# Kernel optimization log

Hardware: AMD Instinct MI355X
Metric: run time of the kernel (lower is better)

The kernel has to match this reference:

```python
import jax, jax.numpy as jnp
import numpy as np

DIM = 192
HEADS = 6
HEAD_DIM = DIM // HEADS
WS = 8
SHIFT = WS // 2
B, H, W = 32, 64, 64
EPS = 1e-5


def _rel_pos_index(ws):
    coords = np.stack(np.meshgrid(np.arange(ws), np.arange(ws), indexing='ij'))  # [2,ws,ws]
    cf = coords.reshape(2, -1)  # [2,N]
    rel = cf[:, :, None] - cf[:, None, :]  # [2,N,N]
    rel = rel.transpose(1, 2, 0)
    rel[:, :, 0] += ws - 1
    rel[:, :, 1] += ws - 1
    rel[:, :, 0] *= 2 * ws - 1
    return jnp.asarray(rel.sum(-1))  # [N,N] int32


def _shift_mask(Hp, Wp, ws, shift):
    img = np.zeros((Hp, Wp))
    slices = (slice(0, -ws), slice(-ws, -shift), slice(-shift, None))
    cnt = 0
    for hs in slices:
        for wsl in slices:
            img[hs, wsl] = cnt
            cnt += 1
    m = img.reshape(Hp // ws, ws, Wp // ws, ws).transpose(0, 2, 1, 3).reshape(-1, ws * ws)
    diff = m[:, None, :] - m[:, :, None]
    return jnp.asarray(np.where(diff != 0, -100.0, 0.0).astype(np.float32))  # [nW,N,N]


def _layernorm(x, g, b):
    mu = x.mean(-1, keepdims=True)
    var = ((x - mu) ** 2).mean(-1, keepdims=True)
    return (x - mu) / jnp.sqrt(var + EPS) * g + b


def _win_part(x, ws):
    b, h, w, c = x.shape
    x = x.reshape(b, h // ws, ws, w // ws, ws, c).transpose(0, 1, 3, 2, 4, 5)
    return x.reshape(-1, ws * ws, c)


def _win_rev(win, ws, h, w):
    b = win.shape[0] // (h * w // ws // ws)
    x = win.reshape(b, h // ws, w // ws, ws, ws, -1).transpose(0, 1, 3, 2, 4, 5)
    return x.reshape(b, h, w, -1)


def setup_inputs() -> dict:
    key = jax.random.key(0)
    ks = jax.random.split(key, 6)
    d = DIM
    init = lambda k, shape, scale: jax.random.normal(k, shape, jnp.float32) * scale
    return {
        'x': jax.random.normal(ks[0], (B, H, W, d), jnp.float32),
        'ln1_g': jnp.ones((d,), jnp.float32),
        'ln1_b': jnp.zeros((d,), jnp.float32),
        'qkv_w': init(ks[1], (3 * d, d), 0.02),
        'qkv_b': jnp.zeros((3 * d,), jnp.float32),
        'proj_w': init(ks[2], (d, d), 0.02),
        'proj_b': jnp.zeros((d,), jnp.float32),
        'rel_bias_table': init(ks[3], ((2 * WS - 1) ** 2, HEADS), 0.02),
        'ln2_g': jnp.ones((d,), jnp.float32),
        'ln2_b': jnp.zeros((d,), jnp.float32),
        'mlp_w1': init(ks[4], (4 * d, d), 0.02),
        'mlp_b1': jnp.zeros((4 * d,), jnp.float32),
        'mlp_w2': init(ks[5], (d, 4 * d), 0.02),
        'mlp_b2': jnp.zeros((d,), jnp.float32),
    }


def reference(x, ln1_g, ln1_b, qkv_w, qkv_b, proj_w, proj_b, rel_bias_table, ln2_g, ln2_b, mlp_w1, mlp_b1, mlp_w2, mlp_b2):
    b, h, w, c = x.shape
    N = WS * WS
    shortcut = x
    y = _layernorm(x, ln1_g, ln1_b)
    # shifted window: roll, partition
    y = jnp.roll(y, shift=(-SHIFT, -SHIFT), axis=(1, 2))
    xw = _win_part(y, WS)  # [B_, N, C]
    B_ = xw.shape[0]
    qkv = (xw @ qkv_w.T + qkv_b).reshape(B_, N, 3, HEADS, HEAD_DIM)
    q, k, v = qkv[:, :, 0], qkv[:, :, 1], qkv[:, :, 2]  # [B_, N, H, hd]
    scale = HEAD_DIM ** -0.5
    attn = jnp.einsum('bnhd,bmhd->bhnm', q * scale, k)  # [B_, H, N, N]
    rel = rel_bias_table[_rel_pos_index(WS)]  # [N, N, heads]
    attn = attn + rel.transpose(2, 0, 1)[None]
    mask = _shift_mask(h, w, WS, SHIFT)  # [nW, N, N]
    nW = mask.shape[0]
    attn = attn.reshape(B_ // nW, nW, HEADS, N, N) + mask[None, :, None]
    attn = jax.nn.softmax(attn.reshape(B_, HEADS, N, N), axis=-1)
    out = jnp.einsum('bhnm,bmhd->bnhd', attn, v).reshape(B_, N, c)
    out = out @ proj_w.T + proj_b
    y = _win_rev(out, WS, h, w)
    y = jnp.roll(y, shift=(SHIFT, SHIFT), axis=(1, 2))
    x2 = shortcut + y
    z = _layernorm(x2, ln2_g, ln2_b)
    z = jax.nn.gelu(z @ mlp_w1.T + mlp_b1, approximate=False) @ mlp_w2.T + mlp_b2
    return x2 + z
```

## Files before the change

### kernel.cpp

```cpp
#include <hip/hip_runtime.h>
#include <hip/hip_bf16.h>

typedef __bf16 bf16_t;
typedef __bf16 bf16x8 __attribute__((ext_vector_type(8)));
typedef float f32x4 __attribute__((ext_vector_type(4)));

#define MFMA16x16(a, b, c) __builtin_amdgcn_mfma_f32_16x16x32_bf16((a), (b), (c), 0, 0, 0)

constexpr int DIM = 192;
constexpr int NHEAD = 6;
constexpr int NWIN = 2048;
constexpr int WTOK = 64;

__global__ __launch_bounds__(256) void cvt_all(const float* __restrict__ qkv,
                                               const float* __restrict__ proj,
                                               const float* __restrict__ w1,
                                               const float* __restrict__ w2,
                                               bf16_t* __restrict__ qkvwf,
                                               bf16_t* __restrict__ pwf,
                                               bf16_t* __restrict__ w1f,
                                               bf16_t* __restrict__ w2f) {
    const int t = blockIdx.x * 256 + threadIdx.x;
    const int lane = t & 63;
    const int r15 = lane & 15, c8 = (lane >> 4) * 8;
    const float* sp;
    bf16_t* dp;
    if (t < 216 * 64) {
        const int f = t >> 6;
        const int nt = f & 1, kk = (f >> 1) % 6, ph = f / 12;
        sp = qkv + (ph * 32 + nt * 16 + r15) * 192 + kk * 32 + c8;
        dp = qkvwf + (size_t)t * 8;
    } else if (t < 288 * 64) {
        const int f = (t >> 6) - 216;
        const int nt = f % 3, kk = (f / 3) % 6, wv = f / 18;
        sp = proj + (wv * 48 + nt * 16 + r15) * 192 + kk * 32 + c8;
        dp = pwf + (size_t)(t - 216 * 64) * 8;
    } else if (t < 576 * 64) {
        const int f = (t >> 6) - 288;
        const int nt = f % 3, kk = (f / 3) % 6, q = f / 18;
        const int wv = q & 3, kc = q >> 2;
        sp = w1 + (kc * 192 + wv * 48 + nt * 16 + r15) * 192 + kk * 32 + c8;
        dp = w1f + (size_t)(t - 288 * 64) * 8;
    } else {
        const int f = (t >> 6) - 576;
        const int nt = f % 3, kk = (f / 3) % 6, q = f / 18;
        const int wv = q & 3, kc = q >> 2;
        sp = w2 + (size_t)(wv * 48 + nt * 16 + r15) * 768 + kc * 192 + kk * 32 + c8;
        dp = w2f + (size_t)(t - 576 * 64) * 8;
    }
#pragma unroll
    for (int e = 0; e < 8; ++e) dp[e] = (bf16_t)sp[e];
}

__global__ __launch_bounds__(256) void ln_win_kernel(const float* __restrict__ in,
                                                     const float* __restrict__ g,
                                                     const float* __restrict__ bta,
                                                     bf16_t* __restrict__ ywf) {
    __shared__ bf16_t y_s[64][200];
    const int tid = threadIdx.x, lane = tid & 63, wv = tid >> 6;
    const int win = blockIdx.x;
    const int b_ = win >> 6, hb = (win >> 3) & 7, wb = win & 7;
    const float gv0 = g[lane], gv1 = g[lane + 64], gv2 = g[lane + 128];
    const float bv0 = bta[lane], bv1 = bta[lane + 64], bv2 = bta[lane + 128];
    for (int i = 0; i < 16; ++i) {
        const int n = wv * 16 + i;
        const int th = n >> 3, tw = n & 7;
        const int hh = (hb * 8 + th + 4) & 63;
        const int ww = (wb * 8 + tw + 4) & 63;
        const size_t src = ((size_t)(b_ * 64 + hh) * 64 + ww) * DIM;
        const float v0 = in[src + lane], v1 = in[src + lane + 64], v2 = in[src + lane + 128];
        float sm = v0 + v1 + v2;
        float q = v0 * v0 + v1 * v1 + v2 * v2;
#pragma unroll
        for (int m = 1; m < 64; m <<= 1) {
            sm += __shfl_xor(sm, m);
            q += __shfl_xor(q, m);
        }
        const float mu = sm * (1.0f / DIM);
        const float inv = rsqrtf(q * (1.0f / DIM) - mu * mu + 1e-5f);
        y_s[n][lane]       = (bf16_t)((v0 - mu) * inv * gv0 + bv0);
        y_s[n][lane + 64]  = (bf16_t)((v1 - mu) * inv * gv1 + bv1);
        y_s[n][lane + 128] = (bf16_t)((v2 - mu) * inv * gv2 + bv2);
    }
    __syncthreads();
    bf16_t* dst = ywf + (size_t)win * 12288;
    for (int j = tid; j < 1536; j += 256) {
        const int f = j >> 6, ln = j & 63;
        const int mt = f & 3, kk = f >> 2;
        const int row = mt * 16 + (ln & 15), col = kk * 32 + (ln >> 4) * 8;
        *reinterpret_cast<bf16x8*>(dst + (size_t)j * 8) =
            *reinterpret_cast<const bf16x8*>(&y_s[row][col]);
    }
}

__global__ __launch_bounds__(64, 3) void attn_kernel(const bf16_t* __restrict__ ywf,
                                                     const bf16_t* __restrict__ qkvwf,
                                                     const float* __restrict__ qkvb,
                                                     const float* __restrict__ relb,
                                                     bf16_t* __restrict__ awf) {
    __shared__ bf16_t scr[6400];
    const int lane = threadIdx.x;
    const int l15 = lane & 15, l4 = lane >> 4;
    const int wh = (blockIdx.x & 7) * ((NWIN * NHEAD) >> 3) + (blockIdx.x >> 3);
    const int win = wh / 6;
    const int h = wh - win * 6;
    const bf16_t* ywin = ywf + (size_t)win * 12288;

    bf16_t* tb = scr;
    bf16_t* vtb = scr + 4096;

    f32x4 aQ[4][2] = {}, aK[4][2] = {}, aV[4][2] = {};
#pragma unroll
    for (int kk = 0; kk < 6; ++kk) {
        bf16x8 a[4];
#pragma unroll
        for (int mt = 0; mt < 4; ++mt)
            a[mt] = *reinterpret_cast<const bf16x8*>(ywin + ((kk * 4 + mt) << 9) + lane * 8);
        bf16x8 bq[2], bk2[2], bv[2];
#pragma unroll
        for (int nt = 0; nt < 2; ++nt) {
            bq[nt] = *reinterpret_cast<const bf16x8*>(
                qkvwf + (size_t)(((((h) * 6 + kk) << 1) + nt) << 9) + lane * 8);
            bk2[nt] = *reinterpret_cast<const bf16x8*>(
                qkvwf + (size_t)(((((6 + h) * 6 + kk) << 1) + nt) << 9) + lane * 8);
            bv[nt] = *reinterpret_cast<const bf16x8*>(
                qkvwf + (size_t)(((((12 + h) * 6 + kk) << 1) + nt) << 9) + lane * 8);
        }
        __builtin_amdgcn_s_setprio(1);
#pragma unroll
        for (int mt = 0; mt < 4; ++mt)
#pragma unroll
            for (int nt = 0; nt < 2; ++nt) {
                aQ[mt][nt] = MFMA16x16(a[mt], bq[nt], aQ[mt][nt]);
                aK[mt][nt] = MFMA16x16(a[mt], bk2[nt], aK[mt][nt]);
                aV[mt][nt] = MFMA16x16(a[mt], bv[nt], aV[mt][nt]);
            }
        __builtin_amdgcn_s_setprio(0);
    }

#pragma unroll
    for (int nt = 0; nt < 2; ++nt) {
        const int d = nt * 16 + l15;
        const float bias = qkvb[(12 + h) * 32 + d];
#pragma unroll
        for (int mt = 0; mt < 4; ++mt)
#pragma unroll
            for (int r = 0; r < 4; ++r)
                vtb[d * 72 + mt * 16 + l4 * 4 + r] = (bf16_t)(aV[mt][nt][r] + bias);
    }
#pragma unroll
    for (int nt = 0; nt < 2; ++nt) {
        const int d = nt * 16 + l15;
        const float bias = qkvb[h * 32 + d];
#pragma unroll
        for (int mt = 0; mt < 4; ++mt)
#pragma unroll
            for (int r = 0; r < 4; ++r)
                tb[(mt * 16 + l4 * 4 + r) * 40 + d] =
                    (bf16_t)((aQ[mt][nt][r] + bias) * 0.17677669529663689f);
    }
    bf16x8 aq[4];
#pragma unroll
    for (int mt = 0; mt < 4; ++mt)
        aq[mt] = *reinterpret_cast<const bf16x8*>(&tb[(mt * 16 + l15) * 40 + l4 * 8]);

#pragma unroll
    for (int nt = 0; nt < 2; ++nt) {
        const int d = nt * 16 + l15;
        const float bias = qkvb[(6 + h) * 32 + d];
#pragma unroll
        for (int mt = 0; mt < 4; ++mt)
#pragma unroll
            for (int r = 0; r < 4; ++r)
                tb[(mt * 16 + l4 * 4 + r) * 40 + d] = (bf16_t)(aK[mt][nt][r] + bias);
    }
    bf16x8 bk[4];
#pragma unroll
    for (int nt = 0; nt < 4; ++nt)
        bk[nt] = *reinterpret_cast<const bf16x8*>(&tb[(nt * 16 + l15) * 40 + l4 * 8]);

    f32x4 s[4][4] = {};
    __builtin_amdgcn_s_setprio(1);
#pragma unroll
    for (int mt = 0; mt < 4; ++mt)
#pragma unroll
        for (int nt = 0; nt < 4; ++nt)
            s[mt][nt] = MFMA16x16(aq[mt], bk[nt], s[mt][nt]);
    __builtin_amdgcn_s_setprio(0);

    const int hb = (win >> 3) & 7, wb = win & 7;
    int colc[4], colreg[4];
#pragma unroll
    for (int nt = 0; nt < 4; ++nt) {
        const int m = nt * 16 + l15;
        const int mh = m >> 3, mw = m & 7;
        colc[nt] = mh * 15 + mw;
        const int gh = hb * 8 + mh, gw = wb * 8 + mw;
        const int rh = (gh < 56) ? 0 : ((gh < 60) ? 1 : 2);
        const int rw = (gw < 56) ? 0 : ((gw < 60) ? 1 : 2);
        colreg[nt] = rh * 3 + rw;
    }
#pragma unroll
    for (int mt = 0; mt < 4; ++mt) {
#pragma unroll
        for (int r = 0; r < 4; ++r) {
            const int n = mt * 16 + l4 * 4 + r;
            const int nh = n >> 3, nw = n & 7;
            const int rowc = nh * 15 + nw + 112;
            const int gh = hb * 8 + nh, gw = wb * 8 + nw;
            const int rh = (gh < 56) ? 0 : ((gh < 60) ? 1 : 2);
            const int rw = (gw < 56) ? 0 : ((gw < 60) ? 1 : 2);
            const int rreg = rh * 3 + rw;
            float vals[4];
            float mx = -1e30f;
#pragma unroll
            for (int nt = 0; nt < 4; ++nt) {
                float v = s[mt][nt][r] + relb[(rowc - colc[nt]) * NHEAD + h];
                if (rreg != colreg[nt]) v -= 100.0f;
                vals[nt] = v;
                mx = fmaxf(mx, v);
            }
            mx = fmaxf(mx, __shfl_xor(mx, 1));
            mx = fmaxf(mx, __shfl_xor(mx, 2));
            mx = fmaxf(mx, __shfl_xor(mx, 4));
            mx = fmaxf(mx, __shfl_xor(mx, 8));
            float sum = 0.f;
#pragma unroll
            for (int nt = 0; nt < 4; ++nt) {
                vals[nt] = __expf(vals[nt] - mx);
                sum += vals[nt];
            }
            sum += __shfl_xor(sum, 1);
            sum += __shfl_xor(sum, 2);
            sum += __shfl_xor(sum, 4);
            sum += __shfl_xor(sum, 8);
            const float inv = 1.0f / sum;
            const int nsw = n & 7;
#pragma unroll
            for (int nt = 0; nt < 4; ++nt) {
                const int tk = nt * 16 + l15;
                tb[n * 64 + (((tk >> 3) ^ nsw) << 3) + (tk & 7)] = (bf16_t)(vals[nt] * inv);
            }
        }
    }

    f32x4 o[4][2] = {};
#pragma unroll
    for (int kk = 0; kk < 2; ++kk) {
        bf16x8 a[4], b[2];
#pragma unroll
        for (int mt = 0; mt < 4; ++mt) {
            const int tq = mt * 16 + l15;
            a[mt] = *reinterpret_cast<const bf16x8*>(&tb[tq * 64 + (((kk * 4 + l4) ^ (tq & 7)) << 3)]);
        }
#pragma unroll
        for (int nt = 0; nt < 2; ++nt)
            b[nt] = *reinterpret_cast<const bf16x8*>(&vtb[(nt * 16 + l15) * 72 + kk * 32 + l4 * 8]);
        __builtin_amdgcn_s_setprio(1);
#pragma unroll
        for (int mt = 0; mt < 4; ++mt)
#pragma unroll
            for (int nt = 0; nt < 2; ++nt)
                o[mt][nt] = MFMA16x16(a[mt], b[nt], o[mt][nt]);
        __builtin_amdgcn_s_setprio(0);
    }

#pragma unroll
    for (int mt = 0; mt < 4; ++mt)
#pragma unroll
        for (int nt = 0; nt < 2; ++nt)
#pragma unroll
            for (int r = 0; r < 4; ++r) {
                const int n = mt * 16 + l4 * 4 + r;
                tb[n * 40 + nt * 16 + l15] = (bf16_t)o[mt][nt][r];
            }
    bf16_t* op = awf + (size_t)win * 12288 + ((size_t)h << 11);
#pragma unroll
    for (int mt = 0; mt < 4; ++mt) {
        const bf16x8 v = *reinterpret_cast<const bf16x8*>(&tb[(mt * 16 + l15) * 40 + l4 * 8]);
        *reinterpret_cast<bf16x8*>(op + (mt << 9) + lane * 8) = v;
    }
}

__global__ __launch_bounds__(256) void proj_kernel(const bf16_t* __restrict__ awf,
                                                   const bf16_t* __restrict__ pwf,
                                                   const float* __restrict__ pbias,
                                                   const float* __restrict__ x,
                                                   float* __restrict__ x2) {
    const int tid = threadIdx.x;
    const int lane = tid & 63;
    const int wv = tid >> 6;
    const int win = blockIdx.x;
    const int l15 = lane & 15, l4 = lane >> 4;
    const bf16_t* awin = awf + (size_t)win * 12288;

    const int n0 = wv * 48;
    f32x4 acc[4][3] = {};
    for (int kk = 0; kk < 6; ++kk) {
        bf16x8 a[4], b[3];
#pragma unroll
        for (int mt = 0; mt < 4; ++mt)
            a[mt] = *reinterpret_cast<const bf16x8*>(awin + ((kk * 4 + mt) << 9) + lane * 8);
#pragma unroll
        for (int nt = 0; nt < 3; ++nt)
            b[nt] = *reinterpret_cast<const bf16x8*>(
                pwf + (size_t)(((wv * 6 + kk) * 3 + nt) << 9) + lane * 8);
#pragma unroll
        for (int mt = 0; mt < 4; ++mt)
#pragma unroll
            for (int nt = 0; nt < 3; ++nt)
                acc[mt][nt] = MFMA16x16(a[mt], b[nt], acc[mt][nt]);
    }
    const int b_ = win >> 6, hb = (win >> 3) & 7, wb = win & 7;
#pragma unroll
    for (int mt = 0; mt < 4; ++mt)
#pragma unroll
        for (int r = 0; r < 4; ++r) {
            const int n = mt * 16 + l4 * 4 + r;
            const int th = n >> 3, tw = n & 7;
            const int hh = (hb * 8 + th + 4) & 63;
            const int ww = (wb * 8 + tw + 4) & 63;
            const size_t row = ((size_t)(b_ * 64 + hh) * 64 + ww) * DIM;
#pragma unroll
            for (int nt = 0; nt < 3; ++nt) {
                const int col = n0 + nt * 16 + l15;
                x2[row + col] = acc[mt][nt][r] + pbias[col] + x[row + col];
            }
        }
}

__device__ __forceinline__ float gelu_f(float v) {
    const float x2 = v * v;
    const float inner = fmaf(0.044715f * x2, v, v);
    const float e = __expf(inner * 1.5957691216057308f);
    const float r = __builtin_amdgcn_rcpf(e + 1.0f);
    return v - v * r;
}

__global__ __launch_bounds__(256, 3) void mlp_kernel(const float* __restrict__ g,
                                                     const float* __restrict__ bta,
                                                     const bf16_t* __restrict__ w1f,
                                                     const float* __restrict__ b1,
                                                     const bf16_t* __restrict__ w2f,
                                                     const float* __restrict__ b2,
                                                     float* __restrict__ xout) {
    __shared__ bf16_t z_s[64][200];
    __shared__ bf16_t h_s[64][200];
    const int tid = threadIdx.x, lane = tid & 63, wv = tid >> 6;
    const int l15 = lane & 15, l4 = lane >> 4;
    const size_t t0 = (size_t)blockIdx.x * 64;
    const int n0 = wv * 48;

    {
        const float gv0 = g[lane], gv1 = g[lane + 64], gv2 = g[lane + 128];
        const float bv0 = bta[lane], bv1 = bta[lane + 64], bv2 = bta[lane + 128];
        for (int i = 0; i < 16; ++i) {
            const int n = wv * 16 + i;
            const size_t src = (t0 + n) * DIM;
            const float v0 = xout[src + lane], v1 = xout[src + lane + 64], v2 = xout[src + lane + 128];
            float sm = v0 + v1 + v2;
            float q = v0 * v0 + v1 * v1 + v2 * v2;
#pragma unroll
            for (int m = 1; m < 64; m <<= 1) {
                sm += __shfl_xor(sm, m);
                q += __shfl_xor(q, m);
            }
            const float mu = sm * (1.0f / DIM);
            const float inv = rsqrtf(q * (1.0f / DIM) - mu * mu + 1e-5f);
            z_s[n][lane]       = (bf16_t)((v0 - mu) * inv * gv0 + bv0);
            z_s[n][lane + 64]  = (bf16_t)((v1 - mu) * inv * gv1 + bv1);
            z_s[n][lane + 128] = (bf16_t)((v2 - mu) * inv * gv2 + bv2);
        }
    }
    __syncthreads();

    f32x4 acc_o[4][3] = {};
    for (int kc = 0; kc < 4; ++kc) {
        const int fb = (kc * 4 + wv) * 18;
        f32x4 hacc[4][3] = {};
#pragma unroll
        for (int kk = 0; kk < 6; ++kk) {
            const int c0 = kk * 32 + l4 * 8;
            bf16x8 a[4], b[3];
#pragma unroll
            for (int mt = 0; mt < 4; ++mt)
                a[mt] = *reinterpret_cast<const bf16x8*>(&z_s[mt * 16 + l15][c0]);
#pragma unroll
            for (int nt = 0; nt < 3; ++nt)
                b[nt] = *reinterpret_cast<const bf16x8*>(
                    w1f + (size_t)((fb + kk * 3 + nt) << 9) + lane * 8);
#pragma unroll
            for (int mt = 0; mt < 4; ++mt)
#pragma unroll
                for (int nt = 0; nt < 3; ++nt)
                    hacc[mt][nt] = MFMA16x16(a[mt], b[nt], hacc[mt][nt]);
        }
        __syncthreads();
#pragma unroll
        for (int mt = 0; mt < 4; ++mt)
#pragma unroll
            for (int r = 0; r < 4; ++r) {
                const int n = mt * 16 + l4 * 4 + r;
#pragma unroll
                for (int nt = 0; nt < 3; ++nt) {
                    const int col = n0 + nt * 16 + l15;
                    h_s[n][col] = (bf16_t)gelu_f(hacc[mt][nt][r] + b1[kc * 192 + col]);
                }
            }
        __syncthreads();
#pragma unroll
        for (int kk = 0; kk < 6; ++kk) {
            const int c0 = kk * 32 + l4 * 8;
            bf16x8 a[4], b[3];
#pragma unroll
            for (int mt = 0; mt < 4; ++mt)
                a[mt] = *reinterpret_cast<const bf16x8*>(&h_s[mt * 16 + l15][c0]);
#pragma unroll
            for (int nt = 0; nt < 3; ++nt)
                b[nt] = *reinterpret_cast<const bf16x8*>(
                    w2f + (size_t)((fb + kk * 3 + nt) << 9) + lane * 8);
#pragma unroll
            for (int mt = 0; mt < 4; ++mt)
#pragma unroll
                for (int nt = 0; nt < 3; ++nt)
                    acc_o[mt][nt] = MFMA16x16(a[mt], b[nt], acc_o[mt][nt]);
        }
    }
#pragma unroll
    for (int mt = 0; mt < 4; ++mt)
#pragma unroll
        for (int r = 0; r < 4; ++r) {
            const int n = mt * 16 + l4 * 4 + r;
            const size_t addr = (t0 + n) * DIM;
#pragma unroll
            for (int nt = 0; nt < 3; ++nt) {
                const int col = n0 + nt * 16 + l15;
                xout[addr + col] = acc_o[mt][nt][r] + b2[col] + xout[addr + col];
            }
        }
}

extern "C" void kernel_launch(void* const* d_in, const int* in_sizes, int n_in,
                              void* d_out, int out_size, void* d_ws, size_t ws_size,
                              hipStream_t stream) {
    const float* x      = (const float*)d_in[0];
    const float* ln1_g  = (const float*)d_in[1];
    const float* ln1_b  = (const float*)d_in[2];
    const float* qkv_w  = (const float*)d_in[3];
    const float* qkv_b  = (const float*)d_in[4];
    const float* proj_w = (const float*)d_in[5];
    const float* proj_b = (const float*)d_in[6];
    const float* relb   = (const float*)d_in[7];
    const float* ln2_g  = (const float*)d_in[8];
    const float* ln2_b  = (const float*)d_in[9];
    const float* mlp_w1 = (const float*)d_in[10];
    const float* mlp_b1 = (const float*)d_in[11];
    const float* mlp_w2 = (const float*)d_in[12];
    const float* mlp_b2 = (const float*)d_in[13];
    float* out = (float*)d_out;

    char* ws = (char*)d_ws;
    bf16_t* qkvwf = (bf16_t*)(ws + 0);
    bf16_t* pwf   = (bf16_t*)(ws + 221184);
    bf16_t* w1f   = (bf16_t*)(ws + 294912);
    bf16_t* w2f   = (bf16_t*)(ws + 589824);
    bf16_t* bufA  = (bf16_t*)(ws + 884736);
    bf16_t* bufB  = (bf16_t*)(ws + 884736 + 50331648);

    cvt_all<<<216, 256, 0, stream>>>(qkv_w, proj_w, mlp_w1, mlp_w2, qkvwf, pwf, w1f, w2f);

    ln_win_kernel<<<NWIN, 256, 0, stream>>>(x, ln1_g, ln1_b, bufA);
    attn_kernel<<<NWIN * NHEAD, 64, 0, stream>>>(bufA, qkvwf, qkv_b, relb, bufB);
    proj_kernel<<<NWIN, 256, 0, stream>>>(bufB, pwf, proj_b, x, out);
    mlp_kernel<<<2048, 256, 0, stream>>>(ln2_g, ln2_b, w1f, mlp_b1, w2f, mlp_b2, out);
}
```

Before: 300.2 us.

## Fuse LayerNorm2 into projection epilogue and feed MLP pre-swizzled bf16 tiles

The projection kernel now computes the post-residual LayerNorm statistics in its epilogue using cross-lane shuffles and a shared-memory reduction over waves. It writes the normalized activations as bf16 in MFMA fragment order to a workspace buffer (reusing bufA). The MLP kernel reads these fragments directly from global memory instead of rereading fp32 x2 and normalizing it, and it works per shifted window with the matching scatter on output. Block-to-window mapping is also swizzled by 8, likely to spread adjacent windows across XCDs or caches. This trades an fp32 reread of x2 for a bf16 write and read, and adds shared memory and a barrier to the projection kernel.

```diff
diff --git a/kernel.cpp b/kernel.cpp
--- a/kernel.cpp
+++ b/kernel.cpp
@@ -282,19 +282,25 @@
     }
 }
 
-__global__ __launch_bounds__(256) void proj_kernel(const bf16_t* __restrict__ awf,
-                                                   const bf16_t* __restrict__ pwf,
-                                                   const float* __restrict__ pbias,
-                                                   const float* __restrict__ x,
-                                                   float* __restrict__ x2) {
+__global__ __launch_bounds__(256) void proj_ln_kernel(const bf16_t* __restrict__ awf,
+                                                      const bf16_t* __restrict__ pwf,
+                                                      const float* __restrict__ pbias,
+                                                      const float* __restrict__ x,
+                                                      const float* __restrict__ g,
+                                                      const float* __restrict__ bta,
+                                                      float* __restrict__ x2,
+                                                      bf16_t* __restrict__ zf) {
+    __shared__ bf16_t z_s[64][200];
+    __shared__ float rsum[64][4];
+    __shared__ float rsq[64][4];
     const int tid = threadIdx.x;
     const int lane = tid & 63;
     const int wv = tid >> 6;
-    const int win = blockIdx.x;
     const int l15 = lane & 15, l4 = lane >> 4;
+    const int win = (blockIdx.x & 7) * (NWIN >> 3) + (blockIdx.x >> 3);
     const bf16_t* awin = awf + (size_t)win * 12288;
-
     const int n0 = wv * 48;
+
     f32x4 acc[4][3] = {};
     for (int kk = 0; kk < 6; ++kk) {
         bf16x8 a[4], b[3];
@@ -321,12 +327,53 @@
             const int hh = (hb * 8 + th + 4) & 63;
             const int ww = (wb * 8 + tw + 4) & 63;
             const size_t row = ((size_t)(b_ * 64 + hh) * 64 + ww) * DIM;
+            float s = 0.f, q = 0.f;
 #pragma unroll
             for (int nt = 0; nt < 3; ++nt) {
                 const int col = n0 + nt * 16 + l15;
-                x2[row + col] = acc[mt][nt][r] + pbias[col] + x[row + col];
-            }
-        }
+                const float v = acc[mt][nt][r] + pbias[col] + x[row + col];
+                acc[mt][nt][r] = v;
+                x2[row + col] = v;
+                s += v;
+                q += v * v;
+            }
+            s += __shfl_xor(s, 1); q += __shfl_xor(q, 1);
+            s += __shfl_xor(s, 2); q += __shfl_xor(q, 2);
+            s += __shfl_xor(s, 4); q += __shfl_xor(q, 4);
+            s += __shfl_xor(s, 8); q += __shfl_xor(q, 8);
+            if (l15 == 0) { rsum[n][wv] = s; rsq[n][wv] = q; }
+        }
+    __syncthreads();
+    float gv[3], bv[3];
+#pragma unroll
+    for (int nt = 0; nt < 3; ++nt) {
+        gv[nt] = g[n0 + nt * 16 + l15];
+        bv[nt] = bta[n0 + nt * 16 + l15];
+    }
+#pragma unroll
+    for (int mt = 0; mt < 4; ++mt)
+#pragma unroll
+        for (int r = 0; r < 4; ++r) {
+            const int n = mt * 16 + l4 * 4 + r;
+            const float s = rsum[n][0] + rsum[n][1] + rsum[n][2] + rsum[n][3];
+            const float q = rsq[n][0] + rsq[n][1] + rsq[n][2] + rsq[n][3];
+            const float mu = s * (1.0f / DIM);
+            const float inv = rsqrtf(q * (1.0f / DIM) - mu * mu + 1e-5f);
+#pragma unroll
+            for (int nt = 0; nt < 3; ++nt) {
+                const int col = n0 + nt * 16 + l15;
+                z_s[n][col] = (bf16_t)((acc[mt][nt][r] - mu) * inv * gv[nt] + bv[nt]);
+            }
+        }
+    __syncthreads();
+    bf16_t* dst = zf + (size_t)win * 12288;
+    for (int j = tid; j < 1536; j += 256) {
+        const int f = j >> 6, ln = j & 63;
+        const int mt = f & 3, kk = f >> 2;
+        const int row = mt * 16 + (ln & 15), col = kk * 32 + (ln >> 4) * 8;
+        *reinterpret_cast<bf16x8*>(dst + (size_t)j * 8) =
+            *reinterpret_cast<const bf16x8*>(&z_s[row][col]);
+    }
 }
 
 __device__ __forceinline__ float gelu_f(float v) {
@@ -337,42 +384,18 @@
     return v - v * r;
 }
 
-__global__ __launch_bounds__(256, 3) void mlp_kernel(const float* __restrict__ g,
-                                                     const float* __restrict__ bta,
+__global__ __launch_bounds__(256, 3) void mlp_kernel(const bf16_t* __restrict__ zf,
                                                      const bf16_t* __restrict__ w1f,
                                                      const float* __restrict__ b1,
                                                      const bf16_t* __restrict__ w2f,
                                                      const float* __restrict__ b2,
                                                      float* __restrict__ xout) {
-    __shared__ bf16_t z_s[64][200];
     __shared__ bf16_t h_s[64][200];
     const int tid = threadIdx.x, lane = tid & 63, wv = tid >> 6;
     const int l15 = lane & 15, l4 = lane >> 4;
-    const size_t t0 = (size_t)blockIdx.x * 64;
+    const int win = (blockIdx.x & 7) * (NWIN >> 3) + (blockIdx.x >> 3);
+    const bf16_t* ztile = zf + (size_t)win * 12288;
     const int n0 = wv * 48;
-
-    {
-        const float gv0 = g[lane], gv1 = g[lane + 64], gv2 = g[lane + 128];
-        const float bv0 = bta[lane], bv1 = bta[lane + 64], bv2 = bta[lane + 128];
-        for (int i = 0; i < 16; ++i) {
-            const int n = wv * 16 + i;
-            const size_t src = (t0 + n) * DIM;
-            const float v0 = xout[src + lane], v1 = xout[src + lane + 64], v2 = xout[src + lane + 128];
-            float sm = v0 + v1 + v2;
-            float q = v0 * v0 + v1 * v1 + v2 * v2;
-#pragma unroll
-            for (int m = 1; m < 64; m <<= 1) {
-                sm += __shfl_xor(sm, m);
-                q += __shfl_xor(q, m);
-            }
-            const float mu = sm * (1.0f / DIM);
-            const float inv = rsqrtf(q * (1.0f / DIM) - mu * mu + 1e-5f);
-            z_s[n][lane]       = (bf16_t)((v0 - mu) * inv * gv0 + bv0);
-            z_s[n][lane + 64]  = (bf16_t)((v1 - mu) * inv * gv1 + bv1);
-            z_s[n][lane + 128] = (bf16_t)((v2 - mu) * inv * gv2 + bv2);
-        }
-    }
-    __syncthreads();
 
     f32x4 acc_o[4][3] = {};
     for (int kc = 0; kc < 4; ++kc) {
@@ -380,11 +403,10 @@
         f32x4 hacc[4][3] = {};
 #pragma unroll
         for (int kk = 0; kk < 6; ++kk) {
-            const int c0 = kk * 32 + l4 * 8;
             bf16x8 a[4], b[3];
 #pragma unroll
             for (int mt = 0; mt < 4; ++mt)
-                a[mt] = *reinterpret_cast<const bf16x8*>(&z_s[mt * 16 + l15][c0]);
+                a[mt] = *reinterpret_cast<const bf16x8*>(ztile + ((kk * 4 + mt) << 9) + lane * 8);
 #pragma unroll
             for (int nt = 0; nt < 3; ++nt)
                 b[nt] = *reinterpret_cast<const bf16x8*>(
@@ -426,12 +448,16 @@
                     acc_o[mt][nt] = MFMA16x16(a[mt], b[nt], acc_o[mt][nt]);
         }
     }
+    const int b_ = win >> 6, hb = (win >> 3) & 7, wb = win & 7;
 #pragma unroll
     for (int mt = 0; mt < 4; ++mt)
 #pragma unroll
         for (int r = 0; r < 4; ++r) {
             const int n = mt * 16 + l4 * 4 + r;
-            const size_t addr = (t0 + n) * DIM;
+            const int th = n >> 3, tw = n & 7;
+            const int hh = (hb * 8 + th + 4) & 63;
+            const int ww = (wb * 8 + tw + 4) & 63;
+            const size_t addr = ((size_t)(b_ * 64 + hh) * 64 + ww) * DIM;
 #pragma unroll
             for (int nt = 0; nt < 3; ++nt) {
                 const int col = n0 + nt * 16 + l15;
@@ -471,6 +497,6 @@
 
     ln_win_kernel<<<NWIN, 256, 0, stream>>>(x, ln1_g, ln1_b, bufA);
     attn_kernel<<<NWIN * NHEAD, 64, 0, stream>>>(bufA, qkvwf, qkv_b, relb, bufB);
-    proj_kernel<<<NWIN, 256, 0, stream>>>(bufB, pwf, proj_b, x, out);
-    mlp_kernel<<<2048, 256, 0, stream>>>(ln2_g, ln2_b, w1f, mlp_b1, w2f, mlp_b2, out);
-}
+    proj_ln_kernel<<<NWIN, 256, 0, stream>>>(bufB, pwf, proj_b, x, ln2_g, ln2_b, out, bufA);
+    mlp_kernel<<<NWIN, 256, 0, stream>>>(bufA, w1f, mlp_b1, w2f, mlp_b2, out);
+}
```

Result: slower. 449.0 us (+49.6%).
